# Kernel optimization log

Measured on AMD Instinct MI355X. Metric: run time of the kernel, lower is better.

The kernel has to match this reference:

```python
import jax, jax.numpy as jnp
import numpy as np

N_NODES = 50000
N_EDGES = 800000
F_IN = 64
HID = 64
N_GRAPHS = 256
BN_EPS = 1e-5


def setup_inputs() -> dict:
    key = jax.random.key(0)
    ks = jax.random.split(key, 16)
    inp = {
        'x': jax.random.normal(ks[0], (N_NODES, F_IN), dtype=jnp.float32),
        'edge_index': jax.random.randint(ks[1], (2, N_EDGES), 0, N_NODES, dtype=jnp.int64),
        'edge_weight': jax.random.uniform(ks[2], (N_EDGES,), dtype=jnp.float32),
        'batch': jnp.sort(jax.random.randint(ks[3], (N_NODES,), 0, N_GRAPHS, dtype=jnp.int64)),
    }
    def lin(k, fi, fo):
        s = 1.0 / np.sqrt(fi)
        kw, kb = jax.random.split(k)
        return (jax.random.uniform(kw, (fi, fo), jnp.float32, -s, s),
                jax.random.uniform(kb, (fo,), jnp.float32, -s, s))
    inp['W1'], inp['b1'] = lin(ks[4], F_IN, HID)
    inp['W2'], inp['b2'] = lin(ks[5], HID, HID)
    inp['W3'], inp['b3'] = lin(ks[6], HID, HID)
    inp['fcW1'], inp['fcb1'] = lin(ks[7], HID, HID)
    inp['fcW2'], inp['fcb2'] = lin(ks[8], HID, 1)
    for i, k in zip((1, 2, 3), ks[9:12]):
        inp[f'g{i}'] = jnp.ones((HID,), jnp.float32)
        inp[f'be{i}'] = jnp.zeros((HID,), jnp.float32)
    return inp


def gin_conv(x, src, dst, edge_weight, W, b):
    # weighted scatter-add aggregation: agg[dst] += w_e * x[src]
    msg = x[src] * edge_weight[:, None]            # [E, d]
    agg = jax.ops.segment_sum(msg, dst, num_segments=x.shape[0])  # [N, d]
    return (x + agg) @ W + b                       # GIN eps=0, nn = Linear


def batch_norm(x, gamma, beta):
    mu = jnp.mean(x, axis=0)
    var = jnp.var(x, axis=0)
    return (x - mu) * jax.lax.rsqrt(var + BN_EPS) * gamma + beta


def reference(x, edge_index, edge_weight, batch,
              W1, b1, W2, b2, W3, b3, fcW1, fcb1, fcW2, fcb2,
              g1, be1, g2, be2, g3, be3):
    src, dst = edge_index[0], edge_index[1]
    h = batch_norm(jax.nn.relu(gin_conv(x, src, dst, edge_weight, W1, b1)), g1, be1)
    h = batch_norm(jax.nn.relu(gin_conv(h, src, dst, edge_weight, W2, b2)), g2, be2)
    h = batch_norm(gin_conv(h, src, dst, edge_weight, W3, b3), g3, be3)
    pooled = jax.ops.segment_sum(h, batch, num_segments=N_GRAPHS)  # global_add_pool
    h = jax.nn.relu(pooled)
    h = jax.nn.relu(h @ fcW1 + fcb1)
    # dropout is identity in eval / deterministic reference
    return (h @ fcW2 + fcb2).reshape(-1)
```

## Files before the change

kernel.cpp:

```cpp
#include <hip/hip_runtime.h>
#include <hip/hip_bf16.h>


#define NN 50000
#define NE 800000
#define FD 64
#define NG 256
#define CAP 64
#define NBKT 16
#define BN_EPS 1e-5f

#define NPART 8
#define PSIZE 6250
#define ECHUNK 2048
#define NCHUNK ((NE + ECHUNK - 1) / ECHUNK)
#define NBUILD (NCHUNK * NPART)
#define NCVT   ((NN * 16) / 256)

__device__ __forceinline__ float4 dec4(uint2 a) {
    float4 f;
    f.x = __uint_as_float(a.x << 16);
    f.y = __uint_as_float(a.x & 0xFFFF0000u);
    f.z = __uint_as_float(a.y << 16);
    f.w = __uint_as_float(a.y & 0xFFFF0000u);
    return f;
}
__device__ __forceinline__ unsigned rbf(float f) {
    unsigned u = __float_as_uint(f);
    return (u + 0x7FFFu + ((u >> 16) & 1u)) >> 16;
}
__device__ __forceinline__ uint2 enc4(float4 v) {
    uint2 o;
    o.x = rbf(v.x) | (rbf(v.y) << 16);
    o.y = rbf(v.z) | (rbf(v.w) << 16);
    return o;
}

__global__ __launch_bounds__(256) void build_cvt_kernel(
    const int* __restrict__ src, const int* __restrict__ dst,
    const float* __restrict__ ew, int* __restrict__ cursor,
    unsigned* __restrict__ slots,
    const float4* __restrict__ xin, uint2* __restrict__ xout)
{
    int bid = blockIdx.x;
    int tid = threadIdx.x;
    if (bid < NBUILD) {
        int part  = bid & 7;
        int chunk = bid >> 3;
        int base  = chunk * ECHUNK;
        #pragma unroll
        for (int i = 0; i < ECHUNK; i += 256) {
            int e = base + i + tid;
            if (e < NE) {
                int d = dst[e];
                if (d / PSIZE == part) {
                    int pos = atomicAdd(&cursor[d], 1) & (CAP - 1);
                    slots[(size_t)d * CAP + pos] =
                        ((unsigned)src[e] << 16) | rbf(ew[e]);
                }
            }
        }
    } else {
        int i = (bid - NBUILD) * 256 + tid;
        xout[i] = enc4(xin[i]);
    }
}

__global__ __launch_bounds__(256) void agg_layer_kernel(
    const uint2* __restrict__ h, const int* __restrict__ deg,
    const unsigned* __restrict__ slots,
    const float* __restrict__ prev_buckets,
    const float* __restrict__ prev_gamma, const float* __restrict__ prev_beta,
    const float* __restrict__ W, const float* __restrict__ b,
    uint2* __restrict__ y, float* __restrict__ buckets, int relu_flag)
{
    __shared__ float Ws[FD * FD];
    __shared__ float ps1[4][FD];
    __shared__ float ps2[4][FD];
    __shared__ float afs[FD], cfs[FD];
    int tid  = threadIdx.x;
    int wave = tid >> 6, lane = tid & 63;
    int g = lane >> 4, l = lane & 15;
    int node = blockIdx.x * 4 + wave;

    {
        float4* Wv = (float4*)Ws;
        const float4* Wg = (const float4*)W;
        #pragma unroll
        for (int i = 0; i < 4; i++) Wv[tid + 256 * i] = Wg[tid + 256 * i];
    }

    unsigned ms = slots[(size_t)node * CAP + lane];
    int dg = deg[node];
    float4 self = dec4(h[(size_t)node * 16 + l]);
    if (dg > CAP) dg = CAP;

    if (prev_buckets) {
        int f = tid & 63, q = tid >> 6;
        float S1 = 0.f, S2 = 0.f;
        #pragma unroll
        for (int i = 0; i < 4; i++) {
            int bkt = q * 4 + i;
            S1 += prev_buckets[bkt * 128 + f];
            S2 += prev_buckets[bkt * 128 + FD + f];
        }
        ps1[q][f] = S1;
        ps2[q][f] = S2;
    }
    __syncthreads();
    if (prev_buckets && tid < FD) {
        float s1 = ps1[0][tid] + ps1[1][tid] + ps1[2][tid] + ps1[3][tid];
        float s2 = ps2[0][tid] + ps2[1][tid] + ps2[2][tid] + ps2[3][tid];
        float mu  = s1 * (1.f / NN);
        float var = s2 * (1.f / NN) - mu * mu;
        float a = prev_gamma[tid] * rsqrtf(var + BN_EPS);
        afs[tid] = a;
        cfs[tid] = prev_beta[tid] - mu * a;
    }
    __syncthreads();

    float4 af = make_float4(1.f, 1.f, 1.f, 1.f);
    float4 cf = make_float4(0.f, 0.f, 0.f, 0.f);
    if (prev_buckets) {
        af = ((const float4*)afs)[l];
        cf = ((const float4*)cfs)[l];
    }

    float4 acc = make_float4(0.f, 0.f, 0.f, 0.f);
    float wsum = 0.f;
    int nIter = (dg + 15) >> 4;
    for (int i = 0; i < nIter; i++) {
        unsigned m[4]; uint2 r[4];
        #pragma unroll
        for (int j = 0; j < 4; j++)
            m[j] = (unsigned)__shfl((int)ms, 16 * i + 4 * j + g, 64);
        #pragma unroll
        for (int j = 0; j < 4; j++)
            r[j] = h[(size_t)(m[j] >> 16) * 16 + l];
        #pragma unroll
        for (int j = 0; j < 4; j++) {
            float w = __uint_as_float(m[j] << 16);
            float4 v = dec4(r[j]);
            wsum += w;
            acc.x = fmaf(w, v.x, acc.x); acc.y = fmaf(w, v.y, acc.y);
            acc.z = fmaf(w, v.z, acc.z); acc.w = fmaf(w, v.w, acc.w);
        }
    }
    acc.x += __shfl_xor(acc.x, 16, 64); acc.y += __shfl_xor(acc.y, 16, 64);
    acc.z += __shfl_xor(acc.z, 16, 64); acc.w += __shfl_xor(acc.w, 16, 64);
    wsum  += __shfl_xor(wsum, 16, 64);
    acc.x += __shfl_xor(acc.x, 32, 64); acc.y += __shfl_xor(acc.y, 32, 64);
    acc.z += __shfl_xor(acc.z, 32, 64); acc.w += __shfl_xor(acc.w, 32, 64);
    wsum  += __shfl_xor(wsum, 32, 64);

    float4 raw;
    raw.x = self.x + acc.x; raw.y = self.y + acc.y;
    raw.z = self.z + acc.z; raw.w = self.w + acc.w;

    float sw = 1.0f + wsum;
    float4 hin;
    hin.x = fmaf(af.x, raw.x, cf.x * sw);
    hin.y = fmaf(af.y, raw.y, cf.y * sw);
    hin.z = fmaf(af.z, raw.z, cf.z * sw);
    hin.w = fmaf(af.w, raw.w, cf.w * sw);

    const float4* __restrict__ WsV = (const float4*)Ws;
    float4 yp = make_float4(0.f, 0.f, 0.f, 0.f);
    #pragma unroll
    for (int kk = 0; kk < 4; kk++) {
        int srcl = 4 * g + kk;
        float a0 = __shfl(hin.x, srcl, 64);
        float a1 = __shfl(hin.y, srcl, 64);
        float a2 = __shfl(hin.z, srcl, 64);
        float a3 = __shfl(hin.w, srcl, 64);
        int k0 = 16 * g + 4 * kk;
        float4 w0 = WsV[(k0 + 0) * 16 + l];
        float4 w1 = WsV[(k0 + 1) * 16 + l];
        float4 w2 = WsV[(k0 + 2) * 16 + l];
        float4 w3 = WsV[(k0 + 3) * 16 + l];
        yp.x = fmaf(a0, w0.x, yp.x); yp.y = fmaf(a0, w0.y, yp.y);
        yp.z = fmaf(a0, w0.z, yp.z); yp.w = fmaf(a0, w0.w, yp.w);
        yp.x = fmaf(a1, w1.x, yp.x); yp.y = fmaf(a1, w1.y, yp.y);
        yp.z = fmaf(a1, w1.z, yp.z); yp.w = fmaf(a1, w1.w, yp.w);
        yp.x = fmaf(a2, w2.x, yp.x); yp.y = fmaf(a2, w2.y, yp.y);
        yp.z = fmaf(a2, w2.z, yp.z); yp.w = fmaf(a2, w2.w, yp.w);
        yp.x = fmaf(a3, w3.x, yp.x); yp.y = fmaf(a3, w3.y, yp.y);
        yp.z = fmaf(a3, w3.z, yp.z); yp.w = fmaf(a3, w3.w, yp.w);
    }
    yp.x += __shfl_xor(yp.x, 16, 64); yp.y += __shfl_xor(yp.y, 16, 64);
    yp.z += __shfl_xor(yp.z, 16, 64); yp.w += __shfl_xor(yp.w, 16, 64);
    yp.x += __shfl_xor(yp.x, 32, 64); yp.y += __shfl_xor(yp.y, 32, 64);
    yp.z += __shfl_xor(yp.z, 32, 64); yp.w += __shfl_xor(yp.w, 32, 64);

    float4 bias = ((const float4*)b)[l];
    float4 yv;
    yv.x = yp.x + bias.x; yv.y = yp.y + bias.y;
    yv.z = yp.z + bias.z; yv.w = yp.w + bias.w;
    if (relu_flag) {
        yv.x = fmaxf(yv.x, 0.f); yv.y = fmaxf(yv.y, 0.f);
        yv.z = fmaxf(yv.z, 0.f); yv.w = fmaxf(yv.w, 0.f);
    }
    if (g == 0) {
        y[(size_t)node * 16 + l] = enc4(yv);
        ((float4*)&ps1[wave][0])[l] = yv;
        float4 sq;
        sq.x = yv.x * yv.x; sq.y = yv.y * yv.y;
        sq.z = yv.z * yv.z; sq.w = yv.w * yv.w;
        ((float4*)&ps2[wave][0])[l] = sq;
    }
    __syncthreads();
    if (tid < FD) {
        float a = ps1[0][tid] + ps1[1][tid] + ps1[2][tid] + ps1[3][tid];
        float q = ps2[0][tid] + ps2[1][tid] + ps2[2][tid] + ps2[3][tid];
        float* bk = buckets + (blockIdx.x & (NBKT - 1)) * 128;
        atomicAdd(&bk[tid], a);
        atomicAdd(&bk[FD + tid], q);
    }
}

__global__ __launch_bounds__(256) void pool_head_kernel(
    const uint2* __restrict__ y, const int* __restrict__ batch,
    const float* __restrict__ buckets3,
    const float* __restrict__ g3, const float* __restrict__ be3,
    const float* __restrict__ fcW1, const float* __restrict__ fcb1,
    const float* __restrict__ fcW2, const float* __restrict__ fcb2,
    float* __restrict__ out)
{
    __shared__ float red[16][FD];
    __shared__ float afs[FD], cfs[FD];
    __shared__ int bounds[2];
    int tid = threadIdx.x;
    int g = blockIdx.x;

    {
        int f = tid & 63, q = tid >> 6;
        float S1 = 0.f, S2 = 0.f;
        #pragma unroll
        for (int i = 0; i < 4; i++) {
            int bkt = q * 4 + i;
            S1 += buckets3[bkt * 128 + f];
            S2 += buckets3[bkt * 128 + FD + f];
        }
        red[q][f]     = S1;
        red[4 + q][f] = S2;
    }
    if (tid < 2) {
        int target = g + tid;
        int lo = 0, hi = NN;
        while (lo < hi) {
            int mid = (lo + hi) >> 1;
            if (batch[mid] < target) lo = mid + 1; else hi = mid;
        }
        bounds[tid] = lo;
    }
    __syncthreads();
    if (tid < FD) {
        float s1 = red[0][tid] + red[1][tid] + red[2][tid] + red[3][tid];
        float s2 = red[4][tid] + red[5][tid] + red[6][tid] + red[7][tid];
        float mu  = s1 * (1.f / NN);
        float var = s2 * (1.f / NN) - mu * mu;
        float a = g3[tid] * rsqrtf(var + BN_EPS);
        afs[tid] = a;
        cfs[tid] = be3[tid] - mu * a;
    }
    __syncthreads();

    int s = bounds[0], e = bounds[1];
    int l = tid & 15, r = tid >> 4;
    float4 acc = make_float4(0.f, 0.f, 0.f, 0.f);
    for (int n = s + r; n < e; n += 16) {
        float4 v = dec4(y[(size_t)n * 16 + l]);
        acc.x += v.x; acc.y += v.y; acc.z += v.z; acc.w += v.w;
    }
    ((float4*)&red[r][0])[l] = acc;
    __syncthreads();
    for (int off = 8; off > 0; off >>= 1) {
        if (r < off) {
            float4 a = ((float4*)&red[r][0])[l];
            float4 o = ((float4*)&red[r + off][0])[l];
            a.x += o.x; a.y += o.y; a.z += o.z; a.w += o.w;
            ((float4*)&red[r][0])[l] = a;
        }
        __syncthreads();
    }
    if (tid < 64) {
        float cnt = (float)(e - s);
        float p = red[0][tid];
        p = fmaf(afs[tid], p, cfs[tid] * cnt);
        p = fmaxf(p, 0.f);
        float acc1 = fcb1[tid];
        #pragma unroll
        for (int k = 0; k < FD; k++) {
            float pk = __shfl(p, k, 64);
            acc1 = fmaf(pk, fcW1[k * FD + tid], acc1);
        }
        acc1 = fmaxf(acc1, 0.f);
        float prod = acc1 * fcW2[tid];
        #pragma unroll
        for (int off = 32; off > 0; off >>= 1)
            prod += __shfl_xor(prod, off, 64);
        if (tid == 0) out[g] = prod + fcb2[0];
    }
}

extern "C" void kernel_launch(void* const* d_in, const int* in_sizes, int n_in,
                              void* d_out, int out_size, void* d_ws, size_t ws_size,
                              hipStream_t stream) {
    const float* x     = (const float*)d_in[0];
    const int*   ei    = (const int*)d_in[1];
    const float* ew    = (const float*)d_in[2];
    const int*   batch = (const int*)d_in[3];
    const float* W1 = (const float*)d_in[4],  *b1 = (const float*)d_in[5];
    const float* W2 = (const float*)d_in[6],  *b2 = (const float*)d_in[7];
    const float* W3 = (const float*)d_in[8],  *b3 = (const float*)d_in[9];
    const float* fcW1 = (const float*)d_in[10], *fcb1 = (const float*)d_in[11];
    const float* fcW2 = (const float*)d_in[12], *fcb2 = (const float*)d_in[13];
    const float* g1 = (const float*)d_in[14], *be1 = (const float*)d_in[15];
    const float* g2 = (const float*)d_in[16], *be2 = (const float*)d_in[17];
    const float* g3 = (const float*)d_in[18], *be3 = (const float*)d_in[19];
    float* out = (float*)d_out;

    const int* srcp = ei;
    const int* dstp = ei + NE;

    char* ws = (char*)d_ws;
    size_t off = 0;
    auto take = [&](size_t bytes) -> char* {
        char* p = ws + off;
        off += (bytes + 255) & ~(size_t)255;
        return p;
    };
    uint2*    xbf   = (uint2*)   take((size_t)NN * FD * 2);
    uint2*    bufA  = (uint2*)   take((size_t)NN * FD * 2);
    uint2*    bufB  = (uint2*)   take((size_t)NN * FD * 2);
    size_t zero_base = off;
    unsigned* slots = (unsigned*)take((size_t)NN * CAP * 4);
    int*      cursor= (int*)     take((size_t)NN * 4);
    float*    buckets=(float*)   take((size_t)3 * NBKT * 128 * 4);
    size_t zero_bytes = off - zero_base;
    (void)ws_size; (void)n_in; (void)in_sizes; (void)out_size;

    hipMemsetAsync(ws + zero_base, 0, zero_bytes, stream);

    build_cvt_kernel<<<NBUILD + NCVT, 256, 0, stream>>>(srcp, dstp, ew,
                                                        cursor, slots,
                                                        (const float4*)x, xbf);

    const int gridA = NN / 4;

    float* bk1 = buckets + 0 * NBKT * 128;
    float* bk2 = buckets + 1 * NBKT * 128;
    float* bk3 = buckets + 2 * NBKT * 128;

    agg_layer_kernel<<<gridA, 256, 0, stream>>>(xbf, cursor, slots,
                                                nullptr, nullptr, nullptr,
                                                W1, b1, bufA, bk1, 1);
    agg_layer_kernel<<<gridA, 256, 0, stream>>>(bufA, cursor, slots,
                                                bk1, g1, be1,
                                                W2, b2, bufB, bk2, 1);
    agg_layer_kernel<<<gridA, 256, 0, stream>>>(bufB, cursor, slots,
                                                bk2, g2, be2,
                                                W3, b3, bufA, bk3, 0);
    pool_head_kernel<<<NG, 256, 0, stream>>>(bufA, batch, bk3, g3, be3,
                                             fcW1, fcb1, fcW2, fcb2, out);
}
```

Measured before the change: 264.1 us.

## Fuse global add pooling into last aggregation layer via atomics

The third GIN layer now accumulates per-graph pooled sums directly with atomicAdd, using the per-wave row values already in shared memory, and no longer writes its output features to global memory. The pool kernel becomes a small head kernel that reads the pooled sums and applies the batch-norm affine fold and the MLP. This removes a full write and re-read of the layer-3 activations and the per-graph reduction pass. In exchange it adds global atomics per block into a 256x64 array, plus nondeterministic float summation order.

```diff
diff --git a/kernel.cpp b/kernel.cpp
--- a/kernel.cpp
+++ b/kernel.cpp
@@ -72,7 +72,8 @@
     const float* __restrict__ prev_buckets,
     const float* __restrict__ prev_gamma, const float* __restrict__ prev_beta,
     const float* __restrict__ W, const float* __restrict__ b,
-    uint2* __restrict__ y, float* __restrict__ buckets, int relu_flag)
+    uint2* __restrict__ y, float* __restrict__ buckets, int relu_flag,
+    const int* __restrict__ batch, float* __restrict__ pooled)
 {
     __shared__ float Ws[FD * FD];
     __shared__ float ps1[4][FD];
@@ -201,7 +202,8 @@
         yv.z = fmaxf(yv.z, 0.f); yv.w = fmaxf(yv.w, 0.f);
     }
     if (g == 0) {
-        y[(size_t)node * 16 + l] = enc4(yv);
+        if (!pooled)
+            y[(size_t)node * 16 + l] = enc4(yv);
         ((float4*)&ps1[wave][0])[l] = yv;
         float4 sq;
         sq.x = yv.x * yv.x; sq.y = yv.y * yv.y;
@@ -215,19 +217,30 @@
         float* bk = buckets + (blockIdx.x & (NBKT - 1)) * 128;
         atomicAdd(&bk[tid], a);
         atomicAdd(&bk[FD + tid], q);
-    }
-}
-
-__global__ __launch_bounds__(256) void pool_head_kernel(
-    const uint2* __restrict__ y, const int* __restrict__ batch,
+        if (pooled) {
+            int n0 = blockIdx.x * 4;
+            int b0 = batch[n0], b3 = batch[n0 + 3];
+            if (b0 == b3) {
+                atomicAdd(&pooled[b0 * FD + tid], a);
+            } else {
+                #pragma unroll
+                for (int w = 0; w < 4; w++)
+                    atomicAdd(&pooled[batch[n0 + w] * FD + tid],
+                              ps1[w][tid]);
+            }
+        }
+    }
+}
+
+__global__ __launch_bounds__(256) void head_kernel(
+    const float* __restrict__ pooled, const int* __restrict__ batch,
     const float* __restrict__ buckets3,
     const float* __restrict__ g3, const float* __restrict__ be3,
     const float* __restrict__ fcW1, const float* __restrict__ fcb1,
     const float* __restrict__ fcW2, const float* __restrict__ fcb2,
     float* __restrict__ out)
 {
-    __shared__ float red[16][FD];
-    __shared__ float afs[FD], cfs[FD];
+    __shared__ float red[8][FD];
     __shared__ int bounds[2];
     int tid = threadIdx.x;
     int g = blockIdx.x;
@@ -254,39 +267,18 @@
         bounds[tid] = lo;
     }
     __syncthreads();
-    if (tid < FD) {
+
+    if (tid < 64) {
         float s1 = red[0][tid] + red[1][tid] + red[2][tid] + red[3][tid];
         float s2 = red[4][tid] + red[5][tid] + red[6][tid] + red[7][tid];
         float mu  = s1 * (1.f / NN);
         float var = s2 * (1.f / NN) - mu * mu;
         float a = g3[tid] * rsqrtf(var + BN_EPS);
-        afs[tid] = a;
-        cfs[tid] = be3[tid] - mu * a;
-    }
-    __syncthreads();
-
-    int s = bounds[0], e = bounds[1];
-    int l = tid & 15, r = tid >> 4;
-    float4 acc = make_float4(0.f, 0.f, 0.f, 0.f);
-    for (int n = s + r; n < e; n += 16) {
-        float4 v = dec4(y[(size_t)n * 16 + l]);
-        acc.x += v.x; acc.y += v.y; acc.z += v.z; acc.w += v.w;
-    }
-    ((float4*)&red[r][0])[l] = acc;
-    __syncthreads();
-    for (int off = 8; off > 0; off >>= 1) {
-        if (r < off) {
-            float4 a = ((float4*)&red[r][0])[l];
-            float4 o = ((float4*)&red[r + off][0])[l];
-            a.x += o.x; a.y += o.y; a.z += o.z; a.w += o.w;
-            ((float4*)&red[r][0])[l] = a;
-        }
-        __syncthreads();
-    }
-    if (tid < 64) {
-        float cnt = (float)(e - s);
-        float p = red[0][tid];
-        p = fmaf(afs[tid], p, cfs[tid] * cnt);
+        float c = be3[tid] - mu * a;
+
+        float cnt = (float)(bounds[1] - bounds[0]);
+        float p = pooled[g * FD + tid];
+        p = fmaf(a, p, c * cnt);
         p = fmaxf(p, 0.f);
         float acc1 = fcb1[tid];
         #pragma unroll
@@ -337,6 +329,7 @@
     unsigned* slots = (unsigned*)take((size_t)NN * CAP * 4);
     int*      cursor= (int*)     take((size_t)NN * 4);
     float*    buckets=(float*)   take((size_t)3 * NBKT * 128 * 4);
+    float*    pooled =(float*)   take((size_t)NG * FD * 4);
     size_t zero_bytes = off - zero_base;
     (void)ws_size; (void)n_in; (void)in_sizes; (void)out_size;
 
@@ -354,13 +347,16 @@
 
     agg_layer_kernel<<<gridA, 256, 0, stream>>>(xbf, cursor, slots,
                                                 nullptr, nullptr, nullptr,
-                                                W1, b1, bufA, bk1, 1);
+                                                W1, b1, bufA, bk1, 1,
+                                                nullptr, nullptr);
     agg_layer_kernel<<<gridA, 256, 0, stream>>>(bufA, cursor, slots,
                                                 bk1, g1, be1,
-                                                W2, b2, bufB, bk2, 1);
+                                                W2, b2, bufB, bk2, 1,
+                                                nullptr, nullptr);
     agg_layer_kernel<<<gridA, 256, 0, stream>>>(bufB, cursor, slots,
                                                 bk2, g2, be2,
-                                                W3, b3, bufA, bk3, 0);
-    pool_head_kernel<<<NG, 256, 0, stream>>>(bufA, batch, bk3, g3, be3,
-                                             fcW1, fcb1, fcW2, fcb2, out);
-}
+                                                W3, b3, bufA, bk3, 0,
+                                                batch, pooled);
+    head_kernel<<<NG, 256, 0, stream>>>(pooled, batch, bk3, g3, be3,
+                                        fcW1, fcb1, fcW2, fcb2, out);
+}
```

New measurement: 261.3 us. No clear change (-1.1%).
